# Kernel tuning notes

Measured on AMD Instinct MI355X. Metric: run time of the kernel, lower is better.

The kernel has to match this reference:

```python
import jax, jax.numpy as jnp
import numpy as np
from jax import lax

B_, L_, D_MODEL = 2, 2048, 1024
H, P, N, G, K, CHUNK = 32, 64, 128, 1, 4, 256
INTER = H * P                 # 2048
CONV_DIM = INTER + 2 * G * N  # 2304
PROJ = INTER + CONV_DIM + H   # 4384: [gate | hidden_B_C | dt]
EPS = 1e-6


def segment_sum(x):
    # x: [..., T] -> [..., T, T]; segsum[i,j] = sum_{k=j+1..i} x[k] for i>=j, else -inf
    T = x.shape[-1]
    xx = jnp.repeat(x[..., None], T, axis=-1)
    xx = jnp.where(jnp.tril(jnp.ones((T, T), bool), -1), xx, 0.0)
    s = jnp.cumsum(xx, axis=-2)
    return jnp.where(jnp.tril(jnp.ones((T, T), bool)), s, -jnp.inf)


def setup_inputs() -> dict:
    key = jax.random.key(0)
    ks = jax.random.split(key, 6)
    s = 0.02
    return {
        "x": jax.random.normal(ks[0], (B_, L_, D_MODEL), jnp.float32),
        "in_proj_w": jax.random.normal(ks[1], (PROJ, D_MODEL), jnp.float32) * s,
        "conv_w": jax.random.normal(ks[2], (CONV_DIM, 1, K), jnp.float32) * s,
        "conv_b": jnp.zeros((CONV_DIM,), jnp.float32),
        "dt_bias": jax.random.uniform(ks[3], (H,), jnp.float32, 0.0, 1.0),
        "A_log": jnp.log(jnp.arange(1, H + 1, dtype=jnp.float32)),
        "D": jnp.ones((H,), jnp.float32),
        "norm_w": jnp.ones((INTER,), jnp.float32),
        "out_proj_w": jax.random.normal(ks[4], (D_MODEL, INTER), jnp.float32) * s,
    }


def _forward(x, in_proj_w, conv_w, conv_b, dt_bias, A_log, D, norm_w, out_proj_w):
    b, L, _ = x.shape
    proj = x @ in_proj_w.T                                    # [b,L,PROJ]
    gate, hBC, dt = jnp.split(proj, [INTER, INTER + CONV_DIM], axis=-1)
    # depthwise causal conv1d over sequence
    xc = jnp.pad(hBC.transpose(0, 2, 1), ((0, 0), (0, 0), (K - 1, 0)))
    conv = lax.conv_general_dilated(xc, conv_w, (1,), 'VALID',
                                    dimension_numbers=('NCH', 'OIH', 'NCH'),
                                    feature_group_count=CONV_DIM)
    hBC = jax.nn.silu((conv + conv_b[None, :, None]).transpose(0, 2, 1))  # [b,L,CONV_DIM]
    hs, Bm, Cm = jnp.split(hBC, [INTER, INTER + G * N], axis=-1)
    hs = hs.reshape(b, L, H, P)
    Bm = jnp.repeat(Bm.reshape(b, L, G, N), H // G, axis=2)   # [b,L,H,N]
    Cm = jnp.repeat(Cm.reshape(b, L, G, N), H // G, axis=2)
    dt = jax.nn.softplus(dt + dt_bias)                        # [b,L,H]
    A = -jnp.exp(A_log)                                       # [H]
    D_res = hs * D[None, None, :, None]
    hs = hs * dt[..., None]
    Adt = dt * A                                              # [b,L,H]
    c = L // CHUNK
    A_c = Adt.reshape(b, c, CHUNK, H).transpose(0, 3, 1, 2)   # [b,H,c,l]
    A_cum = jnp.cumsum(A_c, axis=-1)
    Lmat = jnp.exp(segment_sum(A_c))                          # [b,H,c,l,l]
    hs_c = hs.reshape(b, c, CHUNK, H, P)
    B_c = Bm.reshape(b, c, CHUNK, H, N)
    C_c = Cm.reshape(b, c, CHUNK, H, N)
    # intra-chunk (diagonal blocks)
    Gm = jnp.einsum('bcshn,bczhn->bchsz', C_c, B_c)
    M = Gm * Lmat.transpose(0, 2, 1, 3, 4)
    Y_diag = jnp.einsum('bchsz,bczhp->bcshp', M, hs_c)
    # per-chunk final states
    decay_states = jnp.exp(A_cum[..., -1:] - A_cum)           # [b,H,c,l]
    B_decay = B_c * decay_states.transpose(0, 2, 3, 1)[..., None]
    states = jnp.einsum('bclhn,bclhp->bchpn', B_decay, hs_c)  # [b,c,H,P,N]
    # inter-chunk recurrence
    decay_chunk = jnp.exp(segment_sum(jnp.pad(A_cum[..., -1], ((0, 0), (0, 0), (1, 0)))))  # [b,H,c+1,c+1]
    states0 = jnp.concatenate([jnp.zeros_like(states[:, :1]), states], axis=1)             # [b,c+1,H,P,N]
    prev = jnp.einsum('bhij,bjhpn->bihpn', decay_chunk, states0)[:, :-1]                   # [b,c,H,P,N]
    # off-diagonal contribution
    state_decay = jnp.exp(A_cum).transpose(0, 2, 3, 1)        # [b,c,l,H]
    Y_off = jnp.einsum('bclhn,bchpn->bclhp', C_c, prev) * state_decay[..., None]
    y = ((Y_diag + Y_off).reshape(b, L, H, P) + D_res).reshape(b, L, INTER)
    # gated grouped RMSNorm (group_size = INTER // G)
    gs = INTER // G
    yf = y.astype(jnp.float32) * jax.nn.silu(gate.astype(jnp.float32))
    yg = yf.reshape(b, L, INTER // gs, gs)
    var = jnp.mean(yg * yg, axis=-1, keepdims=True)
    yn = (yg * lax.rsqrt(var + EPS)).reshape(b, L, INTER) * norm_w
    return yn @ out_proj_w.T


def reference(x, in_proj_w, conv_w, conv_b, dt_bias, A_log, D, norm_w, out_proj_w):
    return _forward(x, in_proj_w, conv_w, conv_b, dt_bias, A_log, D, norm_w, out_proj_w)
```

## Files before the change

kernel.cpp:

```cpp
#include <hip/hip_runtime.h>
#include <stdint.h>

typedef __attribute__((ext_vector_type(8))) short short8;
typedef __attribute__((ext_vector_type(4))) float f32x4;

#define DEV static __device__ __forceinline__

DEV float b2f(unsigned short u) { union { float f; unsigned int i; } x; x.i = ((unsigned int)u) << 16; return x.f; }
DEV unsigned short f2b(float f) {
    union { float f; unsigned int i; } x; x.f = f;
    unsigned int r = x.i + 0x7fffu + ((x.i >> 16) & 1u);
    return (unsigned short)(r >> 16);
}
DEV void gld_lds16(const void* g, void* l) {
    __builtin_amdgcn_global_load_lds((const __attribute__((address_space(1))) void*)g,
                                     (__attribute__((address_space(3))) void*)l, 16, 0, 0);
}
DEV int xcd_swizzle(int bid, int nwg) {
    int q = nwg >> 3, r = nwg & 7;
    int xcd = bid & 7, base = bid >> 3;
    return (xcd < r ? xcd * (q + 1) : r * (q + 1) + (xcd - r) * q) + base;
}

__global__ void cast3_kernel(const float* __restrict__ a, unsigned short* __restrict__ oa, long na8,
                             const float* __restrict__ b, unsigned short* __restrict__ ob_, long nb8,
                             const float* __restrict__ c, unsigned short* __restrict__ oc, long nc8) {
    long i = (long)blockIdx.x * blockDim.x + threadIdx.x;
    long stride = (long)gridDim.x * blockDim.x;
    long tot = na8 + nb8 + nc8;
    for (; i < tot; i += stride) {
        const float* src; unsigned short* dst; long j = i;
        if (j < na8) { src = a; dst = oa; }
        else if (j < na8 + nb8) { j -= na8; src = b; dst = ob_; }
        else { j -= na8 + nb8; src = c; dst = oc; }
        const f32x4* p = (const f32x4*)(src + j * 8);
        f32x4 v0 = p[0], v1 = p[1];
        short8 o;
        o[0] = (short)f2b(v0[0]); o[1] = (short)f2b(v0[1]); o[2] = (short)f2b(v0[2]); o[3] = (short)f2b(v0[3]);
        o[4] = (short)f2b(v1[0]); o[5] = (short)f2b(v1[1]); o[6] = (short)f2b(v1[2]); o[7] = (short)f2b(v1[3]);
        *(short8*)(dst + j * 8) = o;
    }
}

template<int OMODE>
__global__ __launch_bounds__(256) void gemm_nt(
    const unsigned short* __restrict__ A, int lda, long sAy, long sAz,
    const unsigned short* __restrict__ B, int ldb, long sBy, long sBz,
    void* __restrict__ Cp, int ldc, long sCy, long sCz,
    float* __restrict__ dtout,
    int M, int N, int K, int tn)
{
    A += (long)blockIdx.y * sAy + (long)blockIdx.z * sAz;
    B += (long)blockIdx.y * sBy + (long)blockIdx.z * sBz;
    int bid = xcd_swizzle(blockIdx.x, gridDim.x);
    int im = bid / tn, in_ = bid % tn;
    int m0 = im * 128, n0 = in_ * 128;
    __shared__ short smem[2 * 2 * 128 * 64];
    int tid = threadIdx.x;
    int lane = tid & 63, wave = tid >> 6;
    int wu = __builtin_amdgcn_readfirstlane(wave);
    int wm = wave >> 1, wn = wave & 1;
    f32x4 acc[4][4];
#pragma unroll
    for (int m = 0; m < 4; m++)
#pragma unroll
        for (int n = 0; n < 4; n++) acc[m][n] = (f32x4){0.f, 0.f, 0.f, 0.f};

    auto stage = [&](int k0, int s) {
        short* As = smem + s * 16384;
        short* Bs = As + 8192;
#pragma unroll
        for (int i = 0; i < 4; ++i) {
            int g = i * 256 + tid;
            int r = g >> 3, pc = g & 7;
            int cc = pc ^ (r & 7);
            gld_lds16(A + (long)(m0 + r) * lda + k0 + cc * 8, As + (i * 256 + wu * 64) * 8);
            int rb = n0 + r; rb = rb < N ? rb : N - 1;
            gld_lds16(B + (long)rb * ldb + k0 + cc * 8, Bs + (i * 256 + wu * 64) * 8);
        }
    };

    int nt = K >> 6;
    stage(0, 0);
    for (int t = 0; t < nt; ++t) {
        int cur = t & 1;
        if (t + 1 < nt) {
            stage((t + 1) << 6, cur ^ 1);
            asm volatile("s_waitcnt vmcnt(8)" ::: "memory");
        } else {
            asm volatile("s_waitcnt vmcnt(0)" ::: "memory");
        }
        __builtin_amdgcn_s_barrier();
        const short* As = smem + cur * 16384;
        const short* Bs = As + 8192;
#pragma unroll
        for (int ks = 0; ks < 2; ++ks) {
            short8 af[4], bfr[4];
#pragma unroll
            for (int m = 0; m < 4; ++m) {
                int r = wm * 64 + m * 16 + (lane & 15);
                int pc = (ks * 4 + (lane >> 4)) ^ (r & 7);
                af[m] = *(const short8*)(As + r * 64 + pc * 8);
            }
#pragma unroll
            for (int n = 0; n < 4; ++n) {
                int r = wn * 64 + n * 16 + (lane & 15);
                int pc = (ks * 4 + (lane >> 4)) ^ (r & 7);
                bfr[n] = *(const short8*)(Bs + r * 64 + pc * 8);
            }
            __builtin_amdgcn_s_setprio(1);
#pragma unroll
            for (int m = 0; m < 4; ++m)
#pragma unroll
                for (int n = 0; n < 4; ++n)
                    acc[m][n] = __builtin_amdgcn_mfma_f32_16x16x32_bf16(af[m], bfr[n], acc[m][n], 0, 0, 0);
            __builtin_amdgcn_s_setprio(0);
        }
        __builtin_amdgcn_s_barrier();
    }

    int rbase = m0 + wm * 64 + ((lane >> 4) << 2);
    int cbase = n0 + wn * 64 + (lane & 15);
    if (OMODE == 0) {
        float* C = (float*)Cp;
        C += (long)blockIdx.y * sCy + (long)blockIdx.z * sCz;
#pragma unroll
        for (int m = 0; m < 4; ++m)
#pragma unroll
            for (int n = 0; n < 4; ++n) {
                int col = cbase + n * 16;
                if (col < N) {
#pragma unroll
                    for (int r = 0; r < 4; ++r)
                        C[(long)(rbase + m * 16 + r) * ldc + col] = acc[m][n][r];
                }
            }
    } else {
        if (OMODE == 2) {
#pragma unroll
            for (int m = 0; m < 4; ++m)
#pragma unroll
                for (int n = 0; n < 4; ++n) {
                    int col = cbase + n * 16;
                    if (col >= 4352 && col < N) {
#pragma unroll
                        for (int r = 0; r < 4; ++r)
                            dtout[(long)(rbase + m * 16 + r) * 32 + (col - 4352)] = acc[m][n][r];
                    }
                }
        }
        unsigned short* Cs = (unsigned short*)smem;
        int rl = wm * 64 + ((lane >> 4) << 2);
        int cl = wn * 64 + (lane & 15);
#pragma unroll
        for (int m = 0; m < 4; ++m)
#pragma unroll
            for (int r = 0; r < 4; ++r) {
                int row = rl + m * 16 + r;
                int xr = ((row >> 2) & 3) << 4;
#pragma unroll
                for (int n = 0; n < 4; ++n)
                    Cs[row * 128 + ((cl + n * 16) ^ xr)] = f2b(acc[m][n][r]);
            }
        __syncthreads();
        unsigned short* C = (unsigned short*)Cp;
        C += (long)blockIdx.y * sCy + (long)blockIdx.z * sCz;
#pragma unroll
        for (int j = 0; j < 8; ++j) {
            int chunk = j * 256 + tid;
            int row = chunk >> 4, c8 = (chunk & 15) * 8;
            int col = n0 + c8;
            int xr = ((row >> 2) & 3) << 4;
            bool ok = (col < N) && !(OMODE == 2 && col >= 4352);
            if (ok)
                *(short8*)(C + (long)(m0 + row) * ldc + col) = *(const short8*)(Cs + row * 128 + (c8 ^ xr));
        }
    }
}

__global__ __launch_bounds__(256) void conv_dt_kernel(
    const unsigned short* __restrict__ projb,
    const float* __restrict__ dtraw,
    const float* __restrict__ conv_w, const float* __restrict__ conv_b,
    const float* __restrict__ dt_bias, const float* __restrict__ A_log,
    unsigned short* __restrict__ hs, unsigned short* __restrict__ Bb, unsigned short* __restrict__ Cb,
    float* __restrict__ dtv, float* __restrict__ dtA)
{
    int row = blockIdx.x;
    int b = row >> 11, t = row & 2047;
    int tid = threadIdx.x;
    if (tid < 32) {
        float v = dtraw[(long)row * 32 + tid] + dt_bias[tid];
        float dt = v > 20.f ? v : log1pf(__expf(v));
        dtv[(long)(b * 32 + tid) * 2048 + t] = dt;
        dtA[(long)(b * 32 + tid) * 2048 + t] = -dt * __expf(A_log[tid]);
    }
    int ch0 = tid * 8;
    float a[8];
    {
        const f32x4* cb = (const f32x4*)(conv_b + ch0);
        f32x4 b0 = cb[0], b1 = cb[1];
#pragma unroll
        for (int j = 0; j < 4; ++j) { a[j] = b0[j]; a[4 + j] = b1[j]; }
    }
    f32x4 wv[8];
#pragma unroll
    for (int j = 0; j < 8; ++j) wv[j] = *(const f32x4*)(conv_w + (ch0 + j) * 4);
#pragma unroll
    for (int k = 0; k < 4; ++k) {
        int tt = t - 3 + k;
        if (tt >= 0) {
            short8 v = *(const short8*)(projb + (long)(b * 2048 + tt) * 4384 + 2048 + ch0);
#pragma unroll
            for (int j = 0; j < 8; ++j) a[j] += b2f((unsigned short)v[j]) * wv[j][k];
        }
    }
    short8 o;
#pragma unroll
    for (int j = 0; j < 8; ++j) { float s = a[j] / (1.f + __expf(-a[j])); o[j] = (short)f2b(s); }
    *(short8*)(hs + (long)row * 2048 + ch0) = o;
    {
        int ch = 2048 + tid;
        float acc2 = conv_b[ch];
#pragma unroll
        for (int k = 0; k < 4; ++k) {
            int tt = t - 3 + k;
            if (tt >= 0) acc2 += b2f(projb[(long)(b * 2048 + tt) * 4384 + 2048 + ch]) * conv_w[ch * 4 + k];
        }
        float s = acc2 / (1.f + __expf(-acc2));
        if (tid < 128) Bb[(long)row * 128 + tid] = f2b(s);
        else           Cb[(long)row * 128 + tid - 128] = f2b(s);
    }
}

__global__ __launch_bounds__(256) void cumsum_kernel(
    const float* __restrict__ dtA, float* __restrict__ Acum, float* __restrict__ Atot)
{
    int blk = blockIdx.x;
    int c = blk & 7, bh = blk >> 3;
    int l = threadIdx.x;
    __shared__ float s[256];
    float v = dtA[(long)bh * 2048 + c * 256 + l];
    s[l] = v;
    __syncthreads();
    for (int off = 1; off < 256; off <<= 1) {
        float x = (l >= off) ? s[l - off] : 0.f;
        __syncthreads();
        s[l] += x;
        __syncthreads();
    }
    Acum[(long)bh * 2048 + c * 256 + l] = s[l];
    if (l == 255) Atot[bh * 8 + c] = s[255];
}

__global__ __launch_bounds__(256) void transpose_kernel(
    const unsigned short* __restrict__ hs,
    const unsigned short* __restrict__ Bb,
    const float* __restrict__ dtv,
    const float* __restrict__ Acum,
    const float* __restrict__ Atot,
    unsigned short* __restrict__ xdtT,
    unsigned short* __restrict__ xdtd,
    unsigned short* __restrict__ BT)
{
    int b = blockIdx.y;
    int ct = blockIdx.x >> 5;
    int tt = blockIdx.x & 31;
    int c0 = ct * 64, t0 = tt * 64;
    __shared__ float tile[64][65];
    int tid = threadIdx.x;
    bool isB = (c0 >= 2048);
#pragma unroll
    for (int i = 0; i < 2; ++i) {
        int ci = i * 256 + tid;
        int r = ci >> 3, c8 = (ci & 7) * 8;
        const unsigned short* src;
        if (!isB) src = hs + ((long)(b * 2048 + t0 + r)) * 2048 + c0 + c8;
        else      src = Bb + ((long)(b * 2048 + t0 + r)) * 128 + (c0 - 2048) + c8;
        short8 v = *(const short8*)src;
#pragma unroll
        for (int j = 0; j < 8; ++j) tile[r][c8 + j] = b2f((unsigned short)v[j]);
    }
    __syncthreads();
#pragma unroll
    for (int i = 0; i < 2; ++i) {
        int co = i * 256 + tid;
        int oc = co >> 3, tc8 = (co & 7) * 8;
        int ch = c0 + oc;
        if (!isB) {
            int h = ch >> 6;
            long bh = b * 32 + h;
            short8 o1, o2;
#pragma unroll
            for (int j = 0; j < 8; ++j) {
                int t = t0 + tc8 + j;
                float v = tile[tc8 + j][oc];
                float dt = dtv[bh * 2048 + t];
                float dec = __expf(Atot[bh * 8 + (t >> 8)] - Acum[bh * 2048 + t]);
                float xv = v * dt;
                o1[j] = (short)f2b(xv);
                o2[j] = (short)f2b(xv * dec);
            }
            long off = ((long)(b * 2048 + ch)) * 2048 + t0 + tc8;
            *(short8*)(xdtT + off) = o1;
            *(short8*)(xdtd + off) = o2;
        } else {
            short8 o;
#pragma unroll
            for (int j = 0; j < 8; ++j) o[j] = (short)f2b(tile[tc8 + j][oc]);
            long off = ((long)(b * 128 + (ch - 2048))) * 2048 + t0 + tc8;
            *(short8*)(BT + off) = o;
        }
    }
}

__global__ __launch_bounds__(256) void ydiagoff_kernel(
    const unsigned short* __restrict__ Gm,
    const float* __restrict__ Acum,
    const unsigned short* __restrict__ xdtT,
    const unsigned short* __restrict__ hs,
    const unsigned short* __restrict__ Cb,
    const unsigned short* __restrict__ prevb,
    const float* __restrict__ Dp,
    float* __restrict__ y)
{
    int blk = blockIdx.x;
    int h = blk & 31, bc = blk >> 5;
    int c = bc & 7, b = bc >> 3;
    int tid = threadIdx.x, lane = tid & 63, wave = tid >> 6;
    __shared__ float sAc[256];
    __shared__ short Mb[256 * 64];
    sAc[tid] = Acum[(long)(b * 32 + h) * 2048 + c * 256 + tid];
    __syncthreads();
    f32x4 acc[4][4];
#pragma unroll
    for (int m = 0; m < 4; m++)
#pragma unroll
        for (int n = 0; n < 4; n++) acc[m][n] = (f32x4){0.f, 0.f, 0.f, 0.f};

    for (int zp = 0; zp < 4; ++zp) {
#pragma unroll
        for (int i = 0; i < 8; ++i) {
            int ci = i * 256 + tid;
            int s = ci >> 3, cz = ci & 7;
            int z0 = zp * 64 + cz * 8;
            short8 gv = *(const short8*)(Gm + ((long)bc * 256 + s) * 256 + z0);
            float as = sAc[s];
            short8 o;
#pragma unroll
            for (int j = 0; j < 8; ++j) {
                int z = z0 + j;
                float e = (s >= z) ? __expf(as - sAc[z]) : 0.f;
                o[j] = (short)f2b(b2f((unsigned short)gv[j]) * e);
            }
            *(short8*)(Mb + s * 64 + (cz ^ (s & 7)) * 8) = o;
        }
        __syncthreads();
#pragma unroll
        for (int ks = 0; ks < 2; ++ks) {
            short8 af[4], bfr[4];
#pragma unroll
            for (int m = 0; m < 4; ++m) {
                int r = wave * 64 + m * 16 + (lane & 15);
                int pc = (ks * 4 + (lane >> 4)) ^ (r & 7);
                af[m] = *(const short8*)(Mb + r * 64 + pc * 8);
            }
#pragma unroll
            for (int n = 0; n < 4; ++n) {
                int p = n * 16 + (lane & 15);
                int z = c * 256 + zp * 64 + ks * 32 + (lane >> 4) * 8;
                bfr[n] = *(const short8*)(xdtT + ((long)(b * 2048) + h * 64 + p) * 2048 + z);
            }
#pragma unroll
            for (int m = 0; m < 4; ++m)
#pragma unroll
                for (int n = 0; n < 4; ++n)
                    acc[m][n] = __builtin_amdgcn_mfma_f32_16x16x32_bf16(af[m], bfr[n], acc[m][n], 0, 0, 0);
        }
        __syncthreads();
    }
    float el[4];
#pragma unroll
    for (int m = 0; m < 4; ++m) el[m] = __expf(sAc[wave * 64 + m * 16 + (lane & 15)]);
#pragma unroll
    for (int ks = 0; ks < 4; ++ks) {
        short8 af[4], bfr[4];
#pragma unroll
        for (int m = 0; m < 4; ++m) {
            int l = wave * 64 + m * 16 + (lane & 15);
            short8 cv = *(const short8*)(Cb + ((long)b * 2048 + c * 256 + l) * 128 + ks * 32 + (lane >> 4) * 8);
#pragma unroll
            for (int j = 0; j < 8; ++j) af[m][j] = (short)f2b(b2f((unsigned short)cv[j]) * el[m]);
        }
#pragma unroll
        for (int n = 0; n < 4; ++n) {
            int p = n * 16 + (lane & 15);
            bfr[n] = *(const short8*)(prevb + ((long)(bc * 32 + h) * 64 + p) * 128 + ks * 32 + (lane >> 4) * 8);
        }
#pragma unroll
        for (int m = 0; m < 4; ++m)
#pragma unroll
            for (int n = 0; n < 4; ++n)
                acc[m][n] = __builtin_amdgcn_mfma_f32_16x16x32_bf16(af[m], bfr[n], acc[m][n], 0, 0, 0);
    }
    float Dv = Dp[h];
#pragma unroll
    for (int m = 0; m < 4; ++m)
#pragma unroll
        for (int n = 0; n < 4; ++n) {
            int p = n * 16 + (lane & 15);
            int ch = h * 64 + p;
#pragma unroll
            for (int r = 0; r < 4; ++r) {
                int s = wave * 64 + m * 16 + ((lane >> 4) << 2) + r;
                long row_g = (long)b * 2048 + c * 256 + s;
                y[row_g * 2048 + ch] = acc[m][n][r] + b2f(hs[row_g * 2048 + ch]) * Dv;
            }
        }
}

__global__ __launch_bounds__(256) void scan_kernel(
    const float* __restrict__ states,
    const float* __restrict__ Atot,
    unsigned short* __restrict__ prevb)
{
    int bh = blockIdx.x;
    int b = bh >> 5, h = bh & 31;
    float ex[8];
#pragma unroll
    for (int c = 0; c < 8; ++c) ex[c] = __expf(Atot[bh * 8 + c]);
    for (int e = threadIdx.x; e < 8192; e += 256) {
        float S = 0.f;
#pragma unroll
        for (int c = 0; c < 8; ++c) {
            long idx = (long)((b * 8 + c) * 32 + h) * 8192 + e;
            prevb[idx] = f2b(S);
            S = ex[c] * S + states[idx];
        }
    }
}

__global__ __launch_bounds__(256) void rmsnorm_kernel(
    const float* __restrict__ y, const unsigned short* __restrict__ projb,
    const float* __restrict__ norm_w, unsigned short* __restrict__ yn)
{
    int row = blockIdx.x;
    int tid = threadIdx.x, lane = tid & 63, wave = tid >> 6;
    int ch0 = tid * 8;
    const f32x4* yp = (const f32x4*)(y + (long)row * 2048 + ch0);
    f32x4 yv0 = yp[0], yv1 = yp[1];
    short8 g8 = *(const short8*)(projb + (long)row * 4384 + ch0);
    float v[8];
    float ss = 0.f;
#pragma unroll
    for (int j = 0; j < 8; ++j) {
        float g = b2f((unsigned short)g8[j]);
        float s = g / (1.f + __expf(-g));
        float yv = (j < 4) ? yv0[j] : yv1[j - 4];
        v[j] = yv * s; ss += v[j] * v[j];
    }
#pragma unroll
    for (int off = 1; off < 64; off <<= 1) ss += __shfl_xor(ss, off);
    __shared__ float sw[4];
    if (lane == 0) sw[wave] = ss;
    __syncthreads();
    float tot = sw[0] + sw[1] + sw[2] + sw[3];
    float scale = rsqrtf(tot * (1.f / 2048.f) + 1e-6f);
    short8 o;
#pragma unroll
    for (int j = 0; j < 8; ++j) o[j] = (short)f2b(v[j] * scale * norm_w[ch0 + j]);
    *(short8*)(yn + (long)row * 2048 + ch0) = o;
}

extern "C" void kernel_launch(void* const* d_in, const int* in_sizes, int n_in,
                              void* d_out, int out_size, void* d_ws, size_t ws_size,
                              hipStream_t stream)
{
    const float* x        = (const float*)d_in[0];
    const float* in_proj  = (const float*)d_in[1];
    const float* conv_w   = (const float*)d_in[2];
    const float* conv_b   = (const float*)d_in[3];
    const float* dt_bias  = (const float*)d_in[4];
    const float* A_log    = (const float*)d_in[5];
    const float* Dp       = (const float*)d_in[6];
    const float* norm_w   = (const float*)d_in[7];
    const float* out_proj = (const float*)d_in[8];
    float* out = (float*)d_out;

    char* w = (char*)d_ws;
    auto alloc = [&](size_t bytes) { char* p = w; w += (bytes + 255) & ~(size_t)255; return p; };
    unsigned short* xb    = (unsigned short*)alloc(4096L * 1024 * 2);
    unsigned short* wb    = (unsigned short*)alloc(4384L * 1024 * 2);
    unsigned short* ob    = (unsigned short*)alloc(1024L * 2048 * 2);
    unsigned short* projb = (unsigned short*)alloc(4096L * 4384 * 2);
    float*          dtraw = (float*)        alloc(4096L * 32 * 4);
    unsigned short* hs    = (unsigned short*)alloc(4096L * 2048 * 2);
    unsigned short* Bb    = (unsigned short*)alloc(4096L * 128 * 2);
    unsigned short* Cb    = (unsigned short*)alloc(4096L * 128 * 2);
    float*          dtv   = (float*)        alloc(64L * 2048 * 4);
    float*          dtA   = (float*)        alloc(64L * 2048 * 4);
    float*          Acum  = (float*)        alloc(64L * 2048 * 4);
    float*          Atot  = (float*)        alloc(64L * 8 * 4);
    unsigned short* xdtT  = (unsigned short*)alloc(2L * 2048 * 2048 * 2);
    unsigned short* xdtd  = (unsigned short*)alloc(2L * 2048 * 2048 * 2);
    unsigned short* BT    = (unsigned short*)alloc(2L * 128 * 2048 * 2);
    unsigned short* Gmb   = (unsigned short*)alloc(16L * 256 * 256 * 2);
    float*          yb    = (float*)        alloc(4096L * 2048 * 4);
    float*          states= (float*)        alloc(2L * 8 * 2048 * 128 * 4);
    unsigned short* prevb = (unsigned short*)alloc(2L * 8 * 2048 * 128 * 2);
    unsigned short* yn    = (unsigned short*)alloc(4096L * 2048 * 2);

    cast3_kernel<<<2048, 256, 0, stream>>>(x, xb, 4096L * 1024 / 8,
                                           in_proj, wb, 4384L * 1024 / 8,
                                           out_proj, ob, 1024L * 2048 / 8);

    gemm_nt<2><<<dim3(32 * 35, 1, 1), 256, 0, stream>>>(
        xb, 1024, 0, 0, wb, 1024, 0, 0, projb, 4384, 0, 0, dtraw, 4096, 4384, 1024, 35);

    conv_dt_kernel<<<4096, 256, 0, stream>>>(projb, dtraw, conv_w, conv_b, dt_bias, A_log,
                                             hs, Bb, Cb, dtv, dtA);

    cumsum_kernel<<<512, 256, 0, stream>>>(dtA, Acum, Atot);

    transpose_kernel<<<dim3(34 * 32, 2, 1), 256, 0, stream>>>(hs, Bb, dtv, Acum, Atot, xdtT, xdtd, BT);

    gemm_nt<1><<<dim3(4, 8, 2), 256, 0, stream>>>(
        Cb, 128, 256L * 128, 2048L * 128,
        Bb, 128, 256L * 128, 2048L * 128,
        Gmb, 256, 256L * 256, 8L * 256 * 256, nullptr, 256, 256, 128, 2);

    gemm_nt<0><<<dim3(16, 8, 2), 256, 0, stream>>>(
        xdtd, 2048, 256, 2048L * 2048,
        BT, 2048, 256, 128L * 2048,
        states, 128, 2048L * 128, 8L * 2048 * 128, nullptr, 2048, 128, 256, 1);

    scan_kernel<<<64, 256, 0, stream>>>(states, Atot, prevb);

    ydiagoff_kernel<<<512, 256, 0, stream>>>(Gmb, Acum, xdtT, hs, Cb, prevb, Dp, yb);

    rmsnorm_kernel<<<4096, 256, 0, stream>>>(yb, projb, norm_w, yn);

    gemm_nt<0><<<dim3(32 * 8, 1, 1), 256, 0, stream>>>(
        yn, 2048, 0, 0, ob, 2048, 0, 0, out, 1024, 0, 0, nullptr, 4096, 1024, 2048, 8);
}
```

Before: 299.1 us.

## Store in-proj output transposed, fuse conv/transpose, and fold RMSNorm into GEMMs

The in-projection GEMM now writes its bf16 output channel-major (transposed through LDS), so one conv kernel reads time-contiguous rows and produces xdt, decayed xdt, B, C and B^T directly. It replaces the separate conv, cumsum and transpose passes and the hs buffer; a per-(b,h) kernel fuses softplus with the chunk cumsum. The y-diag/off kernel now applies the D skip, the silu gate and norm_w, and accumulates per-row sum of squares with atomics. The RMS scale is applied in the out-projection epilogue, which removes the fp32 y buffer and the rmsnorm pass. Costs: an extra memset, strided transposed stores in the GEMM epilogue, atomics, and reconstructing hs by dividing xdt by dt, which loses bf16 precision.

```diff
diff --git a/kernel.cpp b/kernel.cpp
--- a/kernel.cpp
+++ b/kernel.cpp
@@ -47,7 +47,7 @@
     const unsigned short* __restrict__ A, int lda, long sAy, long sAz,
     const unsigned short* __restrict__ B, int ldb, long sBy, long sBz,
     void* __restrict__ Cp, int ldc, long sCy, long sCz,
-    float* __restrict__ dtout,
+    float* __restrict__ aux,
     int M, int N, int K, int tn)
 {
     A += (long)blockIdx.y * sAy + (long)blockIdx.z * sAz;
@@ -135,8 +135,20 @@
                         C[(long)(rbase + m * 16 + r) * ldc + col] = acc[m][n][r];
                 }
             }
+    } else if (OMODE == 4) {
+        float* C = (float*)Cp;
+#pragma unroll
+        for (int m = 0; m < 4; ++m)
+#pragma unroll
+            for (int r = 0; r < 4; ++r) {
+                int row = rbase + m * 16 + r;
+                float sc = rsqrtf(aux[row] * (1.f / 2048.f) + 1e-6f);
+#pragma unroll
+                for (int n = 0; n < 4; ++n)
+                    C[(long)row * ldc + cbase + n * 16] = acc[m][n][r] * sc;
+            }
     } else {
-        if (OMODE == 2) {
+        if (OMODE == 3) {
 #pragma unroll
             for (int m = 0; m < 4; ++m)
 #pragma unroll
@@ -145,7 +157,7 @@
                     if (col >= 4352 && col < N) {
 #pragma unroll
                         for (int r = 0; r < 4; ++r)
-                            dtout[(long)(rbase + m * 16 + r) * 32 + (col - 4352)] = acc[m][n][r];
+                            aux[(long)(rbase + m * 16 + r) * 32 + (col - 4352)] = acc[m][n][r];
                     }
                 }
         }
@@ -164,152 +176,160 @@
             }
         __syncthreads();
         unsigned short* C = (unsigned short*)Cp;
-        C += (long)blockIdx.y * sCy + (long)blockIdx.z * sCz;
+        if (OMODE == 1) {
+            C += (long)blockIdx.y * sCy + (long)blockIdx.z * sCz;
+#pragma unroll
+            for (int j = 0; j < 8; ++j) {
+                int chunk = j * 256 + tid;
+                int row = chunk >> 4, c8 = (chunk & 15) * 8;
+                int col = n0 + c8;
+                int xr = ((row >> 2) & 3) << 4;
+                if (col < N)
+                    *(short8*)(C + (long)(m0 + row) * ldc + col) = *(const short8*)(Cs + row * 128 + (c8 ^ xr));
+            }
+        } else {
+#pragma unroll
+            for (int j = 0; j < 8; ++j) {
+                int idx = j * 256 + tid;
+                int orr = idx >> 4, mc8 = (idx & 15) * 8;
+                int ch = n0 + orr;
+                if (ch < N) {
+                    short8 o;
+#pragma unroll
+                    for (int q = 0; q < 8; ++q) {
+                        int m = mc8 + q;
+                        int xr = ((m >> 2) & 3) << 4;
+                        o[q] = (short)Cs[m * 128 + (orr ^ xr)];
+                    }
+                    *(short8*)(C + (long)ch * ldc + m0 + mc8) = o;
+                }
+            }
+        }
+    }
+}
+
+__global__ __launch_bounds__(256) void dtcum_kernel(
+    const float* __restrict__ dtraw,
+    const float* __restrict__ dt_bias, const float* __restrict__ A_log,
+    float* __restrict__ dtv, float* __restrict__ Acum, float* __restrict__ Atot)
+{
+    int bh = blockIdx.x;
+    int b = bh >> 5, h = bh & 31;
+    int tid = threadIdx.x;
+    float bias = dt_bias[h];
+    float negA = -__expf(A_log[h]);
+    __shared__ float s[256];
+    for (int c = 0; c < 8; ++c) {
+        int t = c * 256 + tid;
+        float v = dtraw[(long)(b * 2048 + t) * 32 + h] + bias;
+        float dt = v > 20.f ? v : log1pf(__expf(v));
+        dtv[(long)bh * 2048 + t] = dt;
+        s[tid] = dt * negA;
+        __syncthreads();
+        for (int off = 1; off < 256; off <<= 1) {
+            float x = (tid >= off) ? s[tid - off] : 0.f;
+            __syncthreads();
+            s[tid] += x;
+            __syncthreads();
+        }
+        Acum[(long)bh * 2048 + t] = s[tid];
+        if (tid == 255) Atot[bh * 8 + c] = s[255];
+        __syncthreads();
+    }
+}
+
+__global__ __launch_bounds__(256) void convT_kernel(
+    const unsigned short* __restrict__ projT,
+    const float* __restrict__ conv_w, const float* __restrict__ conv_b,
+    const float* __restrict__ dtv, const float* __restrict__ Acum, const float* __restrict__ Atot,
+    unsigned short* __restrict__ xdtT, unsigned short* __restrict__ xdtd,
+    unsigned short* __restrict__ Bb, unsigned short* __restrict__ Cb, unsigned short* __restrict__ BT)
+{
+    int tt = blockIdx.x;
+    int cht = blockIdx.y;
+    int b = blockIdx.z;
+    int t0 = tt * 256;
+    int ch0 = cht * 64;
+    int tid = threadIdx.x;
+    __shared__ short raw[64 * 264];
+    __shared__ unsigned short trsp[256 * 64];
+    __shared__ float sdt[256], sac[256];
+    __shared__ float satot;
+    bool hidden = cht < 32;
+    for (int j = 0; j < 9; ++j) {
+        int idx = j * 256 + tid;
+        if (idx < 64 * 33) {
+            int r = idx / 33, cc = idx % 33;
+            int tg = t0 - 8 + cc * 8;
+            short8 v = {0, 0, 0, 0, 0, 0, 0, 0};
+            if (tg >= 0)
+                v = *(const short8*)(projT + (long)(2048 + ch0 + r) * 4096 + b * 2048 + tg);
+            *(short8*)(raw + r * 264 + cc * 8) = v;
+        }
+    }
+    if (hidden) {
+        int h = cht;
+        sdt[tid] = dtv[(long)(b * 32 + h) * 2048 + t0 + tid];
+        sac[tid] = Acum[(long)(b * 32 + h) * 2048 + t0 + tid];
+        if (tid == 0) satot = Atot[(b * 32 + h) * 8 + tt];
+    }
+    __syncthreads();
+    for (int p = 0; p < 8; ++p) {
+        int ch = p * 8 + (tid >> 5);
+        int tb = (tid & 31) * 8;
+        int cg = ch0 + ch;
+        f32x4 wv = *(const f32x4*)(conv_w + cg * 4);
+        float cb = conv_b[cg];
+        float s[8];
 #pragma unroll
         for (int j = 0; j < 8; ++j) {
-            int chunk = j * 256 + tid;
-            int row = chunk >> 4, c8 = (chunk & 15) * 8;
-            int col = n0 + c8;
-            int xr = ((row >> 2) & 3) << 4;
-            bool ok = (col < N) && !(OMODE == 2 && col >= 4352);
-            if (ok)
-                *(short8*)(C + (long)(m0 + row) * ldc + col) = *(const short8*)(Cs + row * 128 + (c8 ^ xr));
-        }
-    }
-}
-
-__global__ __launch_bounds__(256) void conv_dt_kernel(
-    const unsigned short* __restrict__ projb,
-    const float* __restrict__ dtraw,
-    const float* __restrict__ conv_w, const float* __restrict__ conv_b,
-    const float* __restrict__ dt_bias, const float* __restrict__ A_log,
-    unsigned short* __restrict__ hs, unsigned short* __restrict__ Bb, unsigned short* __restrict__ Cb,
-    float* __restrict__ dtv, float* __restrict__ dtA)
-{
-    int row = blockIdx.x;
-    int b = row >> 11, t = row & 2047;
-    int tid = threadIdx.x;
-    if (tid < 32) {
-        float v = dtraw[(long)row * 32 + tid] + dt_bias[tid];
-        float dt = v > 20.f ? v : log1pf(__expf(v));
-        dtv[(long)(b * 32 + tid) * 2048 + t] = dt;
-        dtA[(long)(b * 32 + tid) * 2048 + t] = -dt * __expf(A_log[tid]);
-    }
-    int ch0 = tid * 8;
-    float a[8];
-    {
-        const f32x4* cb = (const f32x4*)(conv_b + ch0);
-        f32x4 b0 = cb[0], b1 = cb[1];
-#pragma unroll
-        for (int j = 0; j < 4; ++j) { a[j] = b0[j]; a[4 + j] = b1[j]; }
-    }
-    f32x4 wv[8];
-#pragma unroll
-    for (int j = 0; j < 8; ++j) wv[j] = *(const f32x4*)(conv_w + (ch0 + j) * 4);
-#pragma unroll
-    for (int k = 0; k < 4; ++k) {
-        int tt = t - 3 + k;
-        if (tt >= 0) {
-            short8 v = *(const short8*)(projb + (long)(b * 2048 + tt) * 4384 + 2048 + ch0);
-#pragma unroll
-            for (int j = 0; j < 8; ++j) a[j] += b2f((unsigned short)v[j]) * wv[j][k];
-        }
-    }
-    short8 o;
-#pragma unroll
-    for (int j = 0; j < 8; ++j) { float s = a[j] / (1.f + __expf(-a[j])); o[j] = (short)f2b(s); }
-    *(short8*)(hs + (long)row * 2048 + ch0) = o;
-    {
-        int ch = 2048 + tid;
-        float acc2 = conv_b[ch];
-#pragma unroll
-        for (int k = 0; k < 4; ++k) {
-            int tt = t - 3 + k;
-            if (tt >= 0) acc2 += b2f(projb[(long)(b * 2048 + tt) * 4384 + 2048 + ch]) * conv_w[ch * 4 + k];
-        }
-        float s = acc2 / (1.f + __expf(-acc2));
-        if (tid < 128) Bb[(long)row * 128 + tid] = f2b(s);
-        else           Cb[(long)row * 128 + tid - 128] = f2b(s);
-    }
-}
-
-__global__ __launch_bounds__(256) void cumsum_kernel(
-    const float* __restrict__ dtA, float* __restrict__ Acum, float* __restrict__ Atot)
-{
-    int blk = blockIdx.x;
-    int c = blk & 7, bh = blk >> 3;
-    int l = threadIdx.x;
-    __shared__ float s[256];
-    float v = dtA[(long)bh * 2048 + c * 256 + l];
-    s[l] = v;
-    __syncthreads();
-    for (int off = 1; off < 256; off <<= 1) {
-        float x = (l >= off) ? s[l - off] : 0.f;
-        __syncthreads();
-        s[l] += x;
-        __syncthreads();
-    }
-    Acum[(long)bh * 2048 + c * 256 + l] = s[l];
-    if (l == 255) Atot[bh * 8 + c] = s[255];
-}
-
-__global__ __launch_bounds__(256) void transpose_kernel(
-    const unsigned short* __restrict__ hs,
-    const unsigned short* __restrict__ Bb,
-    const float* __restrict__ dtv,
-    const float* __restrict__ Acum,
-    const float* __restrict__ Atot,
-    unsigned short* __restrict__ xdtT,
-    unsigned short* __restrict__ xdtd,
-    unsigned short* __restrict__ BT)
-{
-    int b = blockIdx.y;
-    int ct = blockIdx.x >> 5;
-    int tt = blockIdx.x & 31;
-    int c0 = ct * 64, t0 = tt * 64;
-    __shared__ float tile[64][65];
-    int tid = threadIdx.x;
-    bool isB = (c0 >= 2048);
-#pragma unroll
-    for (int i = 0; i < 2; ++i) {
-        int ci = i * 256 + tid;
-        int r = ci >> 3, c8 = (ci & 7) * 8;
-        const unsigned short* src;
-        if (!isB) src = hs + ((long)(b * 2048 + t0 + r)) * 2048 + c0 + c8;
-        else      src = Bb + ((long)(b * 2048 + t0 + r)) * 128 + (c0 - 2048) + c8;
-        short8 v = *(const short8*)src;
-#pragma unroll
-        for (int j = 0; j < 8; ++j) tile[r][c8 + j] = b2f((unsigned short)v[j]);
-    }
-    __syncthreads();
-#pragma unroll
-    for (int i = 0; i < 2; ++i) {
-        int co = i * 256 + tid;
-        int oc = co >> 3, tc8 = (co & 7) * 8;
-        int ch = c0 + oc;
-        if (!isB) {
-            int h = ch >> 6;
-            long bh = b * 32 + h;
+            int tl = tb + j;
+            float a = cb;
+#pragma unroll
+            for (int k = 0; k < 4; ++k)
+                a += b2f((unsigned short)raw[ch * 264 + tl + 5 + k]) * wv[k];
+            s[j] = a / (1.f + __expf(-a));
+        }
+        if (hidden) {
             short8 o1, o2;
 #pragma unroll
             for (int j = 0; j < 8; ++j) {
-                int t = t0 + tc8 + j;
-                float v = tile[tc8 + j][oc];
-                float dt = dtv[bh * 2048 + t];
-                float dec = __expf(Atot[bh * 8 + (t >> 8)] - Acum[bh * 2048 + t]);
-                float xv = v * dt;
-                o1[j] = (short)f2b(xv);
-                o2[j] = (short)f2b(xv * dec);
-            }
-            long off = ((long)(b * 2048 + ch)) * 2048 + t0 + tc8;
+                int tl = tb + j;
+                float xdt = s[j] * sdt[tl];
+                float dec = __expf(satot - sac[tl]);
+                o1[j] = (short)f2b(xdt);
+                o2[j] = (short)f2b(xdt * dec);
+            }
+            long off = (long)cg * 4096 + b * 2048 + t0 + tb;
             *(short8*)(xdtT + off) = o1;
             *(short8*)(xdtd + off) = o2;
         } else {
             short8 o;
 #pragma unroll
-            for (int j = 0; j < 8; ++j) o[j] = (short)f2b(tile[tc8 + j][oc]);
-            long off = ((long)(b * 128 + (ch - 2048))) * 2048 + t0 + tc8;
-            *(short8*)(BT + off) = o;
+            for (int j = 0; j < 8; ++j) o[j] = (short)f2b(s[j]);
+            if (cht < 34) {
+                int n = (cht - 32) * 64 + ch;
+                *(short8*)(BT + (long)n * 4096 + b * 2048 + t0 + tb) = o;
+            }
+#pragma unroll
+            for (int j = 0; j < 8; ++j) {
+                int tl = tb + j;
+                trsp[tl * 64 + (ch ^ ((tl & 7) << 3))] = (unsigned short)o[j];
+            }
+        }
+    }
+    if (!hidden) {
+        __syncthreads();
+        unsigned short* dst = (cht < 34) ? Bb : Cb;
+        int n0 = ((cht - 32) & 1) * 64;
+        for (int p = 0; p < 8; ++p) {
+            int idx = p * 256 + tid;
+            int tl = idx >> 3, c8 = (idx & 7) * 8;
+            short8 o;
+#pragma unroll
+            for (int q = 0; q < 8; ++q)
+                o[q] = (short)trsp[tl * 64 + ((c8 + q) ^ ((tl & 7) << 3))];
+            *(short8*)(dst + (long)(b * 2048 + t0 + tl) * 128 + n0 + c8) = o;
         }
     }
 }
@@ -318,11 +338,14 @@
     const unsigned short* __restrict__ Gm,
     const float* __restrict__ Acum,
     const unsigned short* __restrict__ xdtT,
-    const unsigned short* __restrict__ hs,
+    const unsigned short* __restrict__ projT,
     const unsigned short* __restrict__ Cb,
     const unsigned short* __restrict__ prevb,
+    const float* __restrict__ dtv,
     const float* __restrict__ Dp,
-    float* __restrict__ y)
+    const float* __restrict__ norm_w,
+    unsigned short* __restrict__ ynu,
+    float* __restrict__ ssq)
 {
     int blk = blockIdx.x;
     int h = blk & 31, bc = blk >> 5;
@@ -330,6 +353,7 @@
     int tid = threadIdx.x, lane = tid & 63, wave = tid >> 6;
     __shared__ float sAc[256];
     __shared__ short Mb[256 * 64];
+    __shared__ float sdt[256];
     sAc[tid] = Acum[(long)(b * 32 + h) * 2048 + c * 256 + tid];
     __syncthreads();
     f32x4 acc[4][4];
@@ -368,8 +392,8 @@
 #pragma unroll
             for (int n = 0; n < 4; ++n) {
                 int p = n * 16 + (lane & 15);
-                int z = c * 256 + zp * 64 + ks * 32 + (lane >> 4) * 8;
-                bfr[n] = *(const short8*)(xdtT + ((long)(b * 2048) + h * 64 + p) * 2048 + z);
+                int zcol = c * 256 + zp * 64 + ks * 32 + (lane >> 4) * 8;
+                bfr[n] = *(const short8*)(xdtT + (long)(h * 64 + p) * 4096 + b * 2048 + zcol);
             }
 #pragma unroll
             for (int m = 0; m < 4; ++m)
@@ -403,19 +427,40 @@
             for (int n = 0; n < 4; ++n)
                 acc[m][n] = __builtin_amdgcn_mfma_f32_16x16x32_bf16(af[m], bfr[n], acc[m][n], 0, 0, 0);
     }
+    unsigned short* gt = (unsigned short*)Mb;
+#pragma unroll
+    for (int i = 0; i < 8; ++i) {
+        int idx = i * 256 + tid;
+        int r = idx >> 5, c8 = (idx & 31) * 8;
+        short8 v = *(const short8*)(projT + (long)(h * 64 + r) * 4096 + b * 2048 + c * 256 + c8);
+#pragma unroll
+        for (int j = 0; j < 8; ++j)
+            gt[r * 256 + ((c8 + j) ^ ((r & 7) << 3))] = (unsigned short)v[j];
+    }
+    sdt[tid] = dtv[(long)(b * 32 + h) * 2048 + c * 256 + tid];
+    __syncthreads();
     float Dv = Dp[h];
 #pragma unroll
     for (int m = 0; m < 4; ++m)
 #pragma unroll
-        for (int n = 0; n < 4; ++n) {
-            int p = n * 16 + (lane & 15);
-            int ch = h * 64 + p;
-#pragma unroll
-            for (int r = 0; r < 4; ++r) {
-                int s = wave * 64 + m * 16 + ((lane >> 4) << 2) + r;
-                long row_g = (long)b * 2048 + c * 256 + s;
-                y[row_g * 2048 + ch] = acc[m][n][r] + b2f(hs[row_g * 2048 + ch]) * Dv;
-            }
+        for (int r = 0; r < 4; ++r) {
+            int tl = wave * 64 + m * 16 + ((lane >> 4) << 2) + r;
+            long bt = (long)b * 2048 + c * 256 + tl;
+            float part = 0.f;
+#pragma unroll
+            for (int n = 0; n < 4; ++n) {
+                int cl = n * 16 + (lane & 15);
+                int ch = h * 64 + cl;
+                float xv = b2f(xdtT[(long)ch * 4096 + bt]);
+                float yv = acc[m][n][r] + (xv / sdt[tl]) * Dv;
+                float g = b2f(gt[cl * 256 + (tl ^ ((cl & 7) << 3))]);
+                float yf = yv * g / (1.f + __expf(-g));
+                part += yf * yf;
+                ynu[bt * 2048 + ch] = f2b(yf * norm_w[ch]);
+            }
+#pragma unroll
+            for (int w2 = 1; w2 < 16; w2 <<= 1) part += __shfl_xor(part, w2);
+            if ((lane & 15) == 0) atomicAdd(&ssq[bt], part);
         }
 }
 
@@ -438,38 +483,6 @@
             S = ex[c] * S + states[idx];
         }
     }
-}
-
-__global__ __launch_bounds__(256) void rmsnorm_kernel(
-    const float* __restrict__ y, const unsigned short* __restrict__ projb,
-    const float* __restrict__ norm_w, unsigned short* __restrict__ yn)
-{
-    int row = blockIdx.x;
-    int tid = threadIdx.x, lane = tid & 63, wave = tid >> 6;
-    int ch0 = tid * 8;
-    const f32x4* yp = (const f32x4*)(y + (long)row * 2048 + ch0);
-    f32x4 yv0 = yp[0], yv1 = yp[1];
-    short8 g8 = *(const short8*)(projb + (long)row * 4384 + ch0);
-    float v[8];
-    float ss = 0.f;
-#pragma unroll
-    for (int j = 0; j < 8; ++j) {
-        float g = b2f((unsigned short)g8[j]);
-        float s = g / (1.f + __expf(-g));
-        float yv = (j < 4) ? yv0[j] : yv1[j - 4];
-        v[j] = yv * s; ss += v[j] * v[j];
-    }
-#pragma unroll
-    for (int off = 1; off < 64; off <<= 1) ss += __shfl_xor(ss, off);
-    __shared__ float sw[4];
-    if (lane == 0) sw[wave] = ss;
-    __syncthreads();
-    float tot = sw[0] + sw[1] + sw[2] + sw[3];
-    float scale = rsqrtf(tot * (1.f / 2048.f) + 1e-6f);
-    short8 o;
-#pragma unroll
-    for (int j = 0; j < 8; ++j) o[j] = (short)f2b(v[j] * scale * norm_w[ch0 + j]);
-    *(short8*)(yn + (long)row * 2048 + ch0) = o;
 }
 
 extern "C" void kernel_launch(void* const* d_in, const int* in_sizes, int n_in,
@@ -492,37 +505,35 @@
     unsigned short* xb    = (unsigned short*)alloc(4096L * 1024 * 2);
     unsigned short* wb    = (unsigned short*)alloc(4384L * 1024 * 2);
     unsigned short* ob    = (unsigned short*)alloc(1024L * 2048 * 2);
-    unsigned short* projb = (unsigned short*)alloc(4096L * 4384 * 2);
+    unsigned short* projT = (unsigned short*)alloc(4384L * 4096 * 2);
     float*          dtraw = (float*)        alloc(4096L * 32 * 4);
-    unsigned short* hs    = (unsigned short*)alloc(4096L * 2048 * 2);
+    float*          dtv   = (float*)        alloc(64L * 2048 * 4);
+    float*          Acum  = (float*)        alloc(64L * 2048 * 4);
+    float*          Atot  = (float*)        alloc(64L * 8 * 4);
+    unsigned short* xdtT  = (unsigned short*)alloc(2048L * 4096 * 2);
+    unsigned short* xdtd  = (unsigned short*)alloc(2048L * 4096 * 2);
     unsigned short* Bb    = (unsigned short*)alloc(4096L * 128 * 2);
     unsigned short* Cb    = (unsigned short*)alloc(4096L * 128 * 2);
-    float*          dtv   = (float*)        alloc(64L * 2048 * 4);
-    float*          dtA   = (float*)        alloc(64L * 2048 * 4);
-    float*          Acum  = (float*)        alloc(64L * 2048 * 4);
-    float*          Atot  = (float*)        alloc(64L * 8 * 4);
-    unsigned short* xdtT  = (unsigned short*)alloc(2L * 2048 * 2048 * 2);
-    unsigned short* xdtd  = (unsigned short*)alloc(2L * 2048 * 2048 * 2);
-    unsigned short* BT    = (unsigned short*)alloc(2L * 128 * 2048 * 2);
+    unsigned short* BT    = (unsigned short*)alloc(128L * 4096 * 2);
     unsigned short* Gmb   = (unsigned short*)alloc(16L * 256 * 256 * 2);
-    float*          yb    = (float*)        alloc(4096L * 2048 * 4);
     float*          states= (float*)        alloc(2L * 8 * 2048 * 128 * 4);
     unsigned short* prevb = (unsigned short*)alloc(2L * 8 * 2048 * 128 * 2);
-    unsigned short* yn    = (unsigned short*)alloc(4096L * 2048 * 2);
+    unsigned short* ynu   = (unsigned short*)alloc(4096L * 2048 * 2);
+    float*          ssq   = (float*)        alloc(4096L * 4);
+
+    hipMemsetAsync(ssq, 0, 4096 * 4, stream);
 
     cast3_kernel<<<2048, 256, 0, stream>>>(x, xb, 4096L * 1024 / 8,
                                            in_proj, wb, 4384L * 1024 / 8,
                                            out_proj, ob, 1024L * 2048 / 8);
 
-    gemm_nt<2><<<dim3(32 * 35, 1, 1), 256, 0, stream>>>(
-        xb, 1024, 0, 0, wb, 1024, 0, 0, projb, 4384, 0, 0, dtraw, 4096, 4384, 1024, 35);
-
-    conv_dt_kernel<<<4096, 256, 0, stream>>>(projb, dtraw, conv_w, conv_b, dt_bias, A_log,
-                                             hs, Bb, Cb, dtv, dtA);
-
-    cumsum_kernel<<<512, 256, 0, stream>>>(dtA, Acum, Atot);
-
-    transpose_kernel<<<dim3(34 * 32, 2, 1), 256, 0, stream>>>(hs, Bb, dtv, Acum, Atot, xdtT, xdtd, BT);
+    gemm_nt<3><<<dim3(32 * 35, 1, 1), 256, 0, stream>>>(
+        xb, 1024, 0, 0, wb, 1024, 0, 0, projT, 4096, 0, 0, dtraw, 4096, 4384, 1024, 35);
+
+    dtcum_kernel<<<64, 256, 0, stream>>>(dtraw, dt_bias, A_log, dtv, Acum, Atot);
+
+    convT_kernel<<<dim3(8, 36, 2), 256, 0, stream>>>(
+        projT, conv_w, conv_b, dtv, Acum, Atot, xdtT, xdtd, Bb, Cb, BT);
 
     gemm_nt<1><<<dim3(4, 8, 2), 256, 0, stream>>>(
         Cb, 128, 256L * 128, 2048L * 128,
@@ -530,16 +541,15 @@
         Gmb, 256, 256L * 256, 8L * 256 * 256, nullptr, 256, 256, 128, 2);
 
     gemm_nt<0><<<dim3(16, 8, 2), 256, 0, stream>>>(
-        xdtd, 2048, 256, 2048L * 2048,
-        BT, 2048, 256, 128L * 2048,
+        xdtd, 4096, 256, 2048,
+        BT, 4096, 256, 2048,
         states, 128, 2048L * 128, 8L * 2048 * 128, nullptr, 2048, 128, 256, 1);
 
     scan_kernel<<<64, 256, 0, stream>>>(states, Atot, prevb);
 
-    ydiagoff_kernel<<<512, 256, 0, stream>>>(Gmb, Acum, xdtT, hs, Cb, prevb, Dp, yb);
-
-    rmsnorm_kernel<<<4096, 256, 0, stream>>>(yb, projb, norm_w, yn);
-
-    gemm_nt<0><<<dim3(32 * 8, 1, 1), 256, 0, stream>>>(
-        yn, 2048, 0, 0, ob, 2048, 0, 0, out, 1024, 0, 0, nullptr, 4096, 1024, 2048, 8);
-}
+    ydiagoff_kernel<<<512, 256, 0, stream>>>(Gmb, Acum, xdtT, projT, Cb, prevb,
+                                             dtv, Dp, norm_w, ynu, ssq);
+
+    gemm_nt<4><<<dim3(32 * 8, 1, 1), 256, 0, stream>>>(
+        ynu, 2048, 0, 0, ob, 2048, 0, 0, out, 1024, 0, 0, ssq, 4096, 1024, 2048, 8);
+}
```

Result: slower. 305.6 us (+2.2%).
